# Optimization experiments

Hardware: AMD Instinct MI355X
Metric: run time of the kernel (lower is better)

Reference implementation:

```python
import jax, jax.numpy as jnp
import numpy as np

N, E = 2048, 65536
EMBED, H0, H1 = 64, 128, 128
VOCAB = 625  # 5**k with k=4
SLOPE = 0.01  # F.leaky_relu_ default negative slope


def setup_inputs() -> dict:
    key = jax.random.key(0)
    ks = jax.random.split(key, 20)
    f = jax.random.normal
    return {
        "node_ids": jax.random.randint(ks[0], (N,), 0, VOCAB),
        "edge_index": jax.random.randint(ks[1], (2, E), 0, N),
        "edge_attr": jax.random.uniform(ks[2], (E, 1), dtype=jnp.float32),
        "m": (jax.random.uniform(ks[3], (N, N)) > 0.5).astype(jnp.float32),
        "emb": f(ks[4], (VOCAB, EMBED), dtype=jnp.float32) * 0.1,
        "l0_lin1": f(ks[5], (H0, EMBED + 1), dtype=jnp.float32) * 0.1,
        "l0_lin2": f(ks[6], (H0, H0), dtype=jnp.float32) * 0.1,
        "l0_att_l": f(ks[7], (H0,), dtype=jnp.float32) * 0.1,
        "l0_att_r": f(ks[8], (EMBED,), dtype=jnp.float32) * 0.1,
        "l0_bias": f(ks[9], (H0,), dtype=jnp.float32) * 0.1,
        "l1_lin1": f(ks[10], (H1, H0 + 1), dtype=jnp.float32) * 0.1,
        "l1_lin2": f(ks[11], (H1, H1), dtype=jnp.float32) * 0.1,
        "l1_att_l": f(ks[12], (H1,), dtype=jnp.float32) * 0.1,
        "l1_att_r": f(ks[13], (H0,), dtype=jnp.float32) * 0.1,
        "l1_bias": f(ks[14], (H1,), dtype=jnp.float32) * 0.1,
        "W1": f(ks[15], (20, (EMBED + H0 + H1) * 2), dtype=jnp.float32) * 0.1,
        "b1": f(ks[16], (20,), dtype=jnp.float32) * 0.1,
        "W2": f(ks[17], (20,), dtype=jnp.float32) * 0.1,
        "b2": f(ks[18], (1,), dtype=jnp.float32) * 0.1,
    }


def _segment_softmax(alpha, index, n):
    # numerically-stable softmax over edges grouped by destination node
    amax = jax.ops.segment_max(alpha, index, num_segments=n)
    amax = jnp.where(jnp.isfinite(amax), amax, 0.0)
    e = jnp.exp(alpha - amax[index])
    denom = jax.ops.segment_sum(e, index, num_segments=n)
    return e / (denom[index] + 1e-16)


def _gate_conv(x, src, dst, edge_attr, lin1, lin2, att_l, att_r, bias, n):
    # PyG AttentiveFP GATEConv: message = lin2(leaky_relu(lin1([x_j, e]))) * alpha
    h = jax.nn.leaky_relu(jnp.concatenate([x[src], edge_attr], axis=-1) @ lin1.T, SLOPE)  # [E,out]
    alpha = jax.nn.leaky_relu(h @ att_l + x[dst] @ att_r, SLOPE)  # [E]
    alpha = _segment_softmax(alpha, dst, n)
    msg = (h @ lin2.T) * alpha[:, None]
    return jax.ops.segment_sum(msg, dst, num_segments=n) + bias


def reference(node_ids, edge_index, edge_attr, m, emb,
              l0_lin1, l0_lin2, l0_att_l, l0_att_r, l0_bias,
              l1_lin1, l1_lin2, l1_att_l, l1_att_r, l1_bias,
              W1, b1, W2, b2):
    src, dst = edge_index[0], edge_index[1]
    x = emb[node_ids]  # [N, EMBED]
    h1 = jax.nn.relu(_gate_conv(x, src, dst, edge_attr, l0_lin1, l0_lin2, l0_att_l, l0_att_r, l0_bias, N))
    h2 = jax.nn.relu(_gate_conv(h1, src, dst, edge_attr, l1_lin1, l1_lin2, l1_att_l, l1_att_r, l1_bias, N))
    feat = jnp.concatenate([x, h1, h2], axis=-1)  # [N, C], C = EMBED+H0+H1
    C = feat.shape[-1]
    # 1x1 conv over concat([x_i, x_j]) == split linear: out[c,i,j] = W1[c,:C]@feat[i] + W1[c,C:]@feat[j] + b1[c]
    a = feat @ W1[:, :C].T  # [N, 20] row (i) term
    b = feat @ W1[:, C:].T  # [N, 20] col (j) term
    h = jax.nn.relu(a[:, None, :] + b[None, :, :] + b1)  # [N, N, 20]
    logits = (h @ W2 + b2[0]) * m  # [N, N]; mask multiplies logits as in original
    return jax.nn.softmax(logits, axis=1)
```

## Files before the change

### kernel.cpp

```cpp
#include <hip/hip_runtime.h>
#include <math.h>

#define N 2048
#define E 65536
#define EMBED 64
#define H 128
#define NT 20
#define C3 320
#define CAP 96
#define SLOPE 0.01f

__device__ __forceinline__ float leaky(float x) { return x > 0.f ? x : SLOPE * x; }

__device__ __forceinline__ float wave_sum(float v) {
#pragma unroll
    for (int o = 32; o > 0; o >>= 1) v += __shfl_xor(v, o, 64);
    return v;
}

__global__ __launch_bounds__(256) void k_prep(
    const int* __restrict__ ei, const float* __restrict__ eattr,
    int* __restrict__ cursor, int* __restrict__ srcs, float* __restrict__ eas,
    const float* __restrict__ l1_lin1, float* __restrict__ WT1,
    const float* __restrict__ l0_lin2, float* __restrict__ LT0,
    const float* __restrict__ l1_lin2, float* __restrict__ LT1,
    const int* __restrict__ ids, const float* __restrict__ emb,
    const float* __restrict__ l0_lin1,
    float* __restrict__ x, float* __restrict__ A) {
    int b = blockIdx.x;
    int tid = threadIdx.x;
    if (b < 256) {
        int e = b * 256 + tid;
        int d = ei[E + e];
        int pos = atomicAdd(&cursor[d], 1);
        if (pos < CAP) {
            srcs[d * CAP + pos] = ei[e];
            eas[d * CAP + pos] = eattr[e];
        }
    } else if (b < 448) {
        int j = (b - 256) * 256 + tid;
        if (j < 16384) {
            int c = j >> 7, k = j & 127;
            WT1[j] = l1_lin1[k * (H + 1) + c];
        } else if (j < 32768) {
            int jj = j - 16384; int c = jj >> 7, k = jj & 127;
            LT0[jj] = l0_lin2[k * H + c];
        } else {
            int jj = j - 32768; int c = jj >> 7, k = jj & 127;
            LT1[jj] = l1_lin2[k * H + c];
        }
    } else {
        __shared__ float lw[EMBED][130];
        int n0 = (b - 448) * 8;
        for (int j = tid; j < H * (EMBED + 1); j += 256) {
            int k = j / (EMBED + 1), c = j % (EMBED + 1);
            float v = l0_lin1[j];
            if (c < EMBED) lw[c][k] = v;
        }
        for (int idx = tid; idx < 8 * EMBED; idx += 256) {
            int g = idx >> 6, c = idx & 63;
            x[(n0 + g) * EMBED + c] = emb[ids[n0 + g] * EMBED + c];
        }
        __syncthreads();
        int k = tid & 127, half = tid >> 7;
        const float* xr[4];
#pragma unroll
        for (int it = 0; it < 4; it++) {
            int nn = __builtin_amdgcn_readfirstlane(n0 + 2 * it + half);
            xr[it] = emb + (size_t)ids[nn] * EMBED;
        }
        float acc[4] = {0.f, 0.f, 0.f, 0.f};
#pragma unroll 4
        for (int c = 0; c < EMBED; c++) {
            float wt = lw[c][k];
#pragma unroll
            for (int it = 0; it < 4; it++) acc[it] = fmaf(xr[it][c], wt, acc[it]);
        }
#pragma unroll
        for (int it = 0; it < 4; it++) A[(n0 + 2 * it + half) * H + k] = acc[it];
    }
}

__device__ __forceinline__ void gate_wave(
    int dst, int lane, float xr,
    const float* __restrict__ A,
    float w0, float w1, float attl0, float attl1,
    const int* __restrict__ srcs, const float* __restrict__ eas, int cnt,
    float& out0, float& out1) {
    int c0 = 2 * lane;
    int base = dst * CAP;
    float mmax = -INFINITY, s = 0.f, v0 = 0.f, v1 = 0.f;
    for (int i0 = 0; i0 < cnt; i0 += 8) {
        int nb = cnt - i0; if (nb > 8) nb = 8;
        float h0[8], h1[8], p[8];
#pragma unroll
        for (int e = 0; e < 8; e++) {
            float ea = 0.f; float2 av = make_float2(0.f, 0.f);
            if (e < nb) {
                int sn = srcs[base + i0 + e];
                ea = eas[base + i0 + e];
                av = *(const float2*)&A[sn * H + c0];
            }
            h0[e] = leaky(fmaf(w0, ea, av.x));
            h1[e] = leaky(fmaf(w1, ea, av.y));
            p[e] = h0[e] * attl0 + h1[e] * attl1;
        }
#pragma unroll
        for (int o = 32; o > 0; o >>= 1) {
#pragma unroll
            for (int e = 0; e < 8; e++) p[e] += __shfl_xor(p[e], o, 64);
        }
        float alpha[8];
#pragma unroll
        for (int e = 0; e < 8; e++)
            alpha[e] = (e < nb) ? leaky(p[e] + xr) : -INFINITY;
        float mb = alpha[0];
#pragma unroll
        for (int e = 1; e < 8; e++) mb = fmaxf(mb, alpha[e]);
        float mnew = fmaxf(mmax, mb);
        float scale = __expf(mmax - mnew);
        float sw = 0.f, sv0 = 0.f, sv1 = 0.f;
#pragma unroll
        for (int e = 0; e < 8; e++) {
            float we = __expf(alpha[e] - mnew);
            sw += we;
            sv0 = fmaf(we, h0[e], sv0);
            sv1 = fmaf(we, h1[e], sv1);
        }
        s = fmaf(s, scale, sw);
        v0 = fmaf(v0, scale, sv0);
        v1 = fmaf(v1, scale, sv1);
        mmax = mnew;
    }
    float inv = 1.f / (s + 1e-16f);
    out0 = v0 * inv;
    out1 = v1 * inv;
}

__global__ __launch_bounds__(512) void k_g0(
    const float* __restrict__ x, const float* __restrict__ A0,
    const float* __restrict__ l0_lin1,
    const float* __restrict__ att_l, const float* __restrict__ att_r,
    const int* __restrict__ srcs, const float* __restrict__ eas,
    const int* __restrict__ cursor,
    const float* __restrict__ LT0, const float* __restrict__ b0,
    const float* __restrict__ WT1,
    float* __restrict__ h1, float* __restrict__ A1) {
    __shared__ float agg_s[8][H];
    __shared__ float hs[8][H];
    int n0 = blockIdx.x * 8;
    int tid = threadIdx.x;
    int wv = __builtin_amdgcn_readfirstlane(tid >> 6);
    int lane = tid & 63;
    int c0 = 2 * lane;

    int dst = n0 + wv;
    float xr = wave_sum(x[dst * EMBED + lane] * att_r[lane]);
    float attl0 = att_l[c0], attl1 = att_l[c0 + 1];
    float w0 = l0_lin1[c0 * (EMBED + 1) + EMBED];
    float w1 = l0_lin1[(c0 + 1) * (EMBED + 1) + EMBED];
    int cnt = cursor[dst]; if (cnt > CAP) cnt = CAP;

    float o0, o1;
    gate_wave(dst, lane, xr, A0, w0, w1, attl0, attl1, srcs, eas, cnt, o0, o1);
    agg_s[wv][c0] = o0;
    agg_s[wv][c0 + 1] = o1;
    __syncthreads();

    int k = tid & 127, q = tid >> 7;
    float bk = b0[k];
    float acc0 = bk, acc1 = bk;
#pragma unroll 4
    for (int c = 0; c < H; c++) {
        float wt = LT0[c * H + k];
        acc0 = fmaf(agg_s[q][c], wt, acc0);
        acc1 = fmaf(agg_s[q + 4][c], wt, acc1);
    }
    float hv0 = fmaxf(acc0, 0.f), hv1 = fmaxf(acc1, 0.f);
    h1[(n0 + q) * H + k] = hv0;
    h1[(n0 + q + 4) * H + k] = hv1;
    hs[q][k] = hv0;
    hs[q + 4][k] = hv1;
    __syncthreads();

    float a0 = 0.f, a1 = 0.f;
#pragma unroll 2
    for (int ct = 0; ct < H / 4; ct++) {
        float u0 = WT1[(4 * ct + 0) * H + k];
        float u1 = WT1[(4 * ct + 1) * H + k];
        float u2 = WT1[(4 * ct + 2) * H + k];
        float u3 = WT1[(4 * ct + 3) * H + k];
        float4 f0 = *(const float4*)&hs[q][4 * ct];
        float4 f1 = *(const float4*)&hs[q + 4][4 * ct];
        a0 = fmaf(f0.x, u0, a0); a0 = fmaf(f0.y, u1, a0);
        a0 = fmaf(f0.z, u2, a0); a0 = fmaf(f0.w, u3, a0);
        a1 = fmaf(f1.x, u0, a1); a1 = fmaf(f1.y, u1, a1);
        a1 = fmaf(f1.z, u2, a1); a1 = fmaf(f1.w, u3, a1);
    }
    A1[(n0 + q) * H + k] = a0;
    A1[(n0 + q + 4) * H + k] = a1;
}

__global__ __launch_bounds__(512) void k_g1(
    const float* __restrict__ h1g, const float* __restrict__ A1,
    const float* __restrict__ l1_lin1,
    const float* __restrict__ att_l, const float* __restrict__ att_r,
    const int* __restrict__ srcs, const float* __restrict__ eas,
    const int* __restrict__ cursor,
    const float* __restrict__ LT1, const float* __restrict__ bL1,
    const float* __restrict__ x, const float* __restrict__ W1,
    float* __restrict__ aArr, float* __restrict__ bT) {
    __shared__ float agg_s[8][H];
    __shared__ float feat[8][C3];
    int n0 = blockIdx.x * 8;
    int tid = threadIdx.x;
    int wv = __builtin_amdgcn_readfirstlane(tid >> 6);
    int lane = tid & 63;
    int c0 = 2 * lane;

    int dst = n0 + wv;
    float xr = wave_sum(h1g[dst * H + lane] * att_r[lane] +
                        h1g[dst * H + 64 + lane] * att_r[64 + lane]);
    float attl0 = att_l[c0], attl1 = att_l[c0 + 1];
    float w0 = l1_lin1[c0 * (H + 1) + H];
    float w1 = l1_lin1[(c0 + 1) * (H + 1) + H];
    int cnt = cursor[dst]; if (cnt > CAP) cnt = CAP;

    float o0, o1;
    gate_wave(dst, lane, xr, A1, w0, w1, attl0, attl1, srcs, eas, cnt, o0, o1);
    agg_s[wv][c0] = o0;
    agg_s[wv][c0 + 1] = o1;

    for (int idx = tid; idx < 8 * EMBED; idx += 512) {
        int g = idx >> 6, c = idx & 63;
        feat[g][c] = x[(n0 + g) * EMBED + c];
    }
    for (int idx = tid; idx < 8 * H; idx += 512) {
        int g = idx >> 7, c = idx & 127;
        feat[g][EMBED + c] = h1g[(n0 + g) * H + c];
    }
    __syncthreads();

    int k = tid & 127, q = tid >> 7;
    float bk = bL1[k];
    float acc0 = bk, acc1 = bk;
#pragma unroll 4
    for (int c = 0; c < H; c++) {
        float wt = LT1[c * H + k];
        acc0 = fmaf(agg_s[q][c], wt, acc0);
        acc1 = fmaf(agg_s[q + 4][c], wt, acc1);
    }
    feat[q][EMBED + H + k] = fmaxf(acc0, 0.f);
    feat[q + 4][EMBED + H + k] = fmaxf(acc1, 0.f);
    __syncthreads();

    if (tid < 320) {
        int g = tid / 40, u = tid % 40;
        int t = u % 20, side = u / 20;
        const float* wrow = W1 + t * (2 * C3) + side * C3;
        float s = 0.f;
#pragma unroll 4
        for (int ct = 0; ct < C3 / 4; ct++) {
            float4 fv = *(const float4*)&feat[g][4 * ct];
            float4 wv4 = *(const float4*)&wrow[4 * ct];
            s = fmaf(fv.x, wv4.x, s);
            s = fmaf(fv.y, wv4.y, s);
            s = fmaf(fv.z, wv4.z, s);
            s = fmaf(fv.w, wv4.w, s);
        }
        if (side == 0) aArr[(n0 + g) * NT + t] = s;
        else bT[t * N + (n0 + g)] = s;
    }
}

__global__ __launch_bounds__(256) void k_final(const float* __restrict__ aArr,
                                               const float* __restrict__ bT,
                                               const float* __restrict__ b1,
                                               const float* __restrict__ W2,
                                               const float* __restrict__ b2,
                                               const float* __restrict__ mmat,
                                               float* __restrict__ out) {
    __shared__ float lg[4][N];
    __shared__ float ash[4][NT];
    __shared__ float red[16];
    int i0 = blockIdx.x * 4;
    int tid = threadIdx.x;
    int wv = tid >> 6;
    if (tid < 4 * NT) ash[tid / NT][tid % NT] = aArr[i0 * NT + tid];
    float w2r[NT], b1r[NT];
#pragma unroll
    for (int t = 0; t < NT; t++) { w2r[t] = W2[t]; b1r[t] = b1[t]; }
    float b2v = b2[0];
    __syncthreads();

    float tmax[4] = {-INFINITY, -INFINITY, -INFINITY, -INFINITY};
    for (int j = tid; j < N; j += 256) {
        float bt[NT];
#pragma unroll
        for (int t = 0; t < NT; t++) bt[t] = bT[t * N + j];
#pragma unroll
        for (int g = 0; g < 4; g++) {
            float l = b2v;
#pragma unroll
            for (int t = 0; t < NT; t++)
                l += fmaxf(ash[g][t] + bt[t] + b1r[t], 0.f) * w2r[t];
            l *= mmat[(size_t)(i0 + g) * N + j];
            lg[g][j] = l;
            tmax[g] = fmaxf(tmax[g], l);
        }
    }
#pragma unroll
    for (int g = 0; g < 4; g++) {
#pragma unroll
        for (int o = 32; o > 0; o >>= 1) tmax[g] = fmaxf(tmax[g], __shfl_xor(tmax[g], o, 64));
    }
    if ((tid & 63) == 0) {
#pragma unroll
        for (int g = 0; g < 4; g++) red[wv * 4 + g] = tmax[g];
    }
    __syncthreads();
    float mfin[4];
#pragma unroll
    for (int g = 0; g < 4; g++)
        mfin[g] = fmaxf(fmaxf(red[g], red[4 + g]), fmaxf(red[8 + g], red[12 + g]));
    __syncthreads();

    float ts[4] = {0.f, 0.f, 0.f, 0.f};
    for (int j = tid; j < N; j += 256) {
#pragma unroll
        for (int g = 0; g < 4; g++) {
            float e = __expf(lg[g][j] - mfin[g]);
            lg[g][j] = e;
            ts[g] += e;
        }
    }
#pragma unroll
    for (int g = 0; g < 4; g++) {
#pragma unroll
        for (int o = 32; o > 0; o >>= 1) ts[g] += __shfl_xor(ts[g], o, 64);
    }
    if ((tid & 63) == 0) {
#pragma unroll
        for (int g = 0; g < 4; g++) red[wv * 4 + g] = ts[g];
    }
    __syncthreads();
    float inv[4];
#pragma unroll
    for (int g = 0; g < 4; g++)
        inv[g] = 1.f / (red[g] + red[4 + g] + red[8 + g] + red[12 + g]);

    for (int j = tid; j < N; j += 256) {
#pragma unroll
        for (int g = 0; g < 4; g++)
            out[(size_t)(i0 + g) * N + j] = lg[g][j] * inv[g];
    }
}

extern "C" void kernel_launch(void* const* d_in, const int* in_sizes, int n_in,
                              void* d_out, int out_size, void* d_ws, size_t ws_size,
                              hipStream_t stream) {
    const int*   node_ids = (const int*)d_in[0];
    const int*   ei       = (const int*)d_in[1];
    const float* eattr    = (const float*)d_in[2];
    const float* mmat     = (const float*)d_in[3];
    const float* emb      = (const float*)d_in[4];
    const float* l0_lin1  = (const float*)d_in[5];
    const float* l0_lin2  = (const float*)d_in[6];
    const float* l0_att_l = (const float*)d_in[7];
    const float* l0_att_r = (const float*)d_in[8];
    const float* l0_bias  = (const float*)d_in[9];
    const float* l1_lin1  = (const float*)d_in[10];
    const float* l1_lin2  = (const float*)d_in[11];
    const float* l1_att_l = (const float*)d_in[12];
    const float* l1_att_r = (const float*)d_in[13];
    const float* l1_bias  = (const float*)d_in[14];
    const float* W1       = (const float*)d_in[15];
    const float* b1       = (const float*)d_in[16];
    const float* W2       = (const float*)d_in[17];
    const float* b2       = (const float*)d_in[18];
    float* out = (float*)d_out;

    char* w = (char*)d_ws;
    auto alloc = [&](size_t bytes) {
        char* p = w;
        w += (bytes + 255) & ~(size_t)255;
        return p;
    };
    int*   cursor = (int*)alloc(N * sizeof(int));
    int*   srcs   = (int*)alloc(N * CAP * sizeof(int));
    float* eas    = (float*)alloc(N * CAP * sizeof(float));
    float* x      = (float*)alloc(N * EMBED * sizeof(float));
    float* A0     = (float*)alloc(N * H * sizeof(float));
    float* A1     = (float*)alloc(N * H * sizeof(float));
    float* h1     = (float*)alloc(N * H * sizeof(float));
    float* aArr   = (float*)alloc(N * NT * sizeof(float));
    float* bT     = (float*)alloc(NT * N * sizeof(float));
    float* WT1    = (float*)alloc(H * H * sizeof(float));
    float* LT0    = (float*)alloc(H * H * sizeof(float));
    float* LT1    = (float*)alloc(H * H * sizeof(float));

    hipMemsetAsync(cursor, 0, N * sizeof(int), stream);

    k_prep<<<704, 256, 0, stream>>>(ei, eattr, cursor, srcs, eas,
                                    l1_lin1, WT1, l0_lin2, LT0, l1_lin2, LT1,
                                    node_ids, emb, l0_lin1, x, A0);
    k_g0<<<N / 8, 512, 0, stream>>>(x, A0, l0_lin1, l0_att_l, l0_att_r,
                                    srcs, eas, cursor, LT0, l0_bias, WT1, h1, A1);
    k_g1<<<N / 8, 512, 0, stream>>>(h1, A1, l1_lin1, l1_att_l, l1_att_r,
                                    srcs, eas, cursor, LT1, l1_bias, x, W1, aArr, bT);
    k_final<<<N / 4, 256, 0, stream>>>(aArr, bT, b1, W2, b2, mmat, out);
}
```

Measured before the change: 193.8 us.

## Fuse all stages into one cooperative persistent kernel with grid syncs

Replaces the memset and four separate kernel launches with a single cooperative kernel of 512 blocks, 256 threads each, that separates stages with grid.sync(). Each block now handles 4 nodes instead of 8, and the cursor zeroing moves inside the kernel. The goal is to remove launch overhead and inter-kernel gaps. In exchange it adds grid-wide barrier costs, lowers per-block parallelism, and requires all 512 blocks to be co-resident, with launch_bounds(256,2) used to help that.

```diff
diff --git a/kernel.cpp b/kernel.cpp
--- a/kernel.cpp
+++ b/kernel.cpp
@@ -1,5 +1,8 @@
 #include <hip/hip_runtime.h>
+#include <hip/hip_cooperative_groups.h>
 #include <math.h>
+
+namespace cg = cooperative_groups;
 
 #define N 2048
 #define E 65536
@@ -16,69 +19,6 @@
 #pragma unroll
     for (int o = 32; o > 0; o >>= 1) v += __shfl_xor(v, o, 64);
     return v;
-}
-
-__global__ __launch_bounds__(256) void k_prep(
-    const int* __restrict__ ei, const float* __restrict__ eattr,
-    int* __restrict__ cursor, int* __restrict__ srcs, float* __restrict__ eas,
-    const float* __restrict__ l1_lin1, float* __restrict__ WT1,
-    const float* __restrict__ l0_lin2, float* __restrict__ LT0,
-    const float* __restrict__ l1_lin2, float* __restrict__ LT1,
-    const int* __restrict__ ids, const float* __restrict__ emb,
-    const float* __restrict__ l0_lin1,
-    float* __restrict__ x, float* __restrict__ A) {
-    int b = blockIdx.x;
-    int tid = threadIdx.x;
-    if (b < 256) {
-        int e = b * 256 + tid;
-        int d = ei[E + e];
-        int pos = atomicAdd(&cursor[d], 1);
-        if (pos < CAP) {
-            srcs[d * CAP + pos] = ei[e];
-            eas[d * CAP + pos] = eattr[e];
-        }
-    } else if (b < 448) {
-        int j = (b - 256) * 256 + tid;
-        if (j < 16384) {
-            int c = j >> 7, k = j & 127;
-            WT1[j] = l1_lin1[k * (H + 1) + c];
-        } else if (j < 32768) {
-            int jj = j - 16384; int c = jj >> 7, k = jj & 127;
-            LT0[jj] = l0_lin2[k * H + c];
-        } else {
-            int jj = j - 32768; int c = jj >> 7, k = jj & 127;
-            LT1[jj] = l1_lin2[k * H + c];
-        }
-    } else {
-        __shared__ float lw[EMBED][130];
-        int n0 = (b - 448) * 8;
-        for (int j = tid; j < H * (EMBED + 1); j += 256) {
-            int k = j / (EMBED + 1), c = j % (EMBED + 1);
-            float v = l0_lin1[j];
-            if (c < EMBED) lw[c][k] = v;
-        }
-        for (int idx = tid; idx < 8 * EMBED; idx += 256) {
-            int g = idx >> 6, c = idx & 63;
-            x[(n0 + g) * EMBED + c] = emb[ids[n0 + g] * EMBED + c];
-        }
-        __syncthreads();
-        int k = tid & 127, half = tid >> 7;
-        const float* xr[4];
-#pragma unroll
-        for (int it = 0; it < 4; it++) {
-            int nn = __builtin_amdgcn_readfirstlane(n0 + 2 * it + half);
-            xr[it] = emb + (size_t)ids[nn] * EMBED;
-        }
-        float acc[4] = {0.f, 0.f, 0.f, 0.f};
-#pragma unroll 4
-        for (int c = 0; c < EMBED; c++) {
-            float wt = lw[c][k];
-#pragma unroll
-            for (int it = 0; it < 4; it++) acc[it] = fmaf(xr[it][c], wt, acc[it]);
-        }
-#pragma unroll
-        for (int it = 0; it < 4; it++) A[(n0 + 2 * it + half) * H + k] = acc[it];
-    }
 }
 
 __device__ __forceinline__ void gate_wave(
@@ -137,222 +77,272 @@
     out1 = v1 * inv;
 }
 
-__global__ __launch_bounds__(512) void k_g0(
-    const float* __restrict__ x, const float* __restrict__ A0,
-    const float* __restrict__ l0_lin1,
-    const float* __restrict__ att_l, const float* __restrict__ att_r,
-    const int* __restrict__ srcs, const float* __restrict__ eas,
-    const int* __restrict__ cursor,
-    const float* __restrict__ LT0, const float* __restrict__ b0,
-    const float* __restrict__ WT1,
-    float* __restrict__ h1, float* __restrict__ A1) {
-    __shared__ float agg_s[8][H];
-    __shared__ float hs[8][H];
-    int n0 = blockIdx.x * 8;
+__global__ __launch_bounds__(256, 2) void k_fused(
+    const int* __restrict__ ei, const float* __restrict__ eattr,
+    const int* __restrict__ ids, const float* __restrict__ emb,
+    const float* __restrict__ l0_lin1, const float* __restrict__ l0_att_l,
+    const float* __restrict__ l0_att_r, const float* __restrict__ l0_bias,
+    const float* __restrict__ l1_lin1, const float* __restrict__ l1_att_l,
+    const float* __restrict__ l1_att_r, const float* __restrict__ l1_bias,
+    const float* __restrict__ l0_lin2, const float* __restrict__ l1_lin2,
+    const float* __restrict__ W1, const float* __restrict__ b1,
+    const float* __restrict__ W2, const float* __restrict__ b2,
+    const float* __restrict__ mmat, float* __restrict__ out,
+    int* __restrict__ cursor, int* __restrict__ srcs, float* __restrict__ eas,
+    float* __restrict__ x, float* __restrict__ A0, float* __restrict__ A1,
+    float* __restrict__ h1g, float* __restrict__ WT1, float* __restrict__ LT0,
+    float* __restrict__ LT1, float* __restrict__ aArr, float* __restrict__ bT) {
+    cg::grid_group grid = cg::this_grid();
+    __shared__ float smem[8352];
+    int b = blockIdx.x;
     int tid = threadIdx.x;
-    int wv = __builtin_amdgcn_readfirstlane(tid >> 6);
     int lane = tid & 63;
-    int c0 = 2 * lane;
-
-    int dst = n0 + wv;
-    float xr = wave_sum(x[dst * EMBED + lane] * att_r[lane]);
-    float attl0 = att_l[c0], attl1 = att_l[c0 + 1];
-    float w0 = l0_lin1[c0 * (EMBED + 1) + EMBED];
-    float w1 = l0_lin1[(c0 + 1) * (EMBED + 1) + EMBED];
-    int cnt = cursor[dst]; if (cnt > CAP) cnt = CAP;
-
-    float o0, o1;
-    gate_wave(dst, lane, xr, A0, w0, w1, attl0, attl1, srcs, eas, cnt, o0, o1);
-    agg_s[wv][c0] = o0;
-    agg_s[wv][c0 + 1] = o1;
-    __syncthreads();
-
-    int k = tid & 127, q = tid >> 7;
-    float bk = b0[k];
-    float acc0 = bk, acc1 = bk;
+    int n4 = b * 4;
+
+    {
+        int j = b * 256 + tid;
+        if (j < 2048) cursor[j] = 0;
+        int j2 = j - 2048;
+        if (j2 >= 0 && j2 < 16384) {
+            int c = j2 >> 7, k = j2 & 127;
+            WT1[j2] = l1_lin1[k * (H + 1) + c];
+        } else if (j2 >= 16384 && j2 < 32768) {
+            int jj = j2 - 16384; int c = jj >> 7, k = jj & 127;
+            LT0[jj] = l0_lin2[k * H + c];
+        } else if (j2 >= 32768 && j2 < 49152) {
+            int jj = j2 - 32768; int c = jj >> 7, k = jj & 127;
+            LT1[jj] = l1_lin2[k * H + c];
+        }
+        float* lw = smem;
+        for (int jj = tid; jj < H * (EMBED + 1); jj += 256) {
+            int k = jj / (EMBED + 1), c = jj % (EMBED + 1);
+            float v = l0_lin1[jj];
+            if (c < EMBED) lw[c * 130 + k] = v;
+        }
+        for (int idx = tid; idx < 4 * EMBED; idx += 256) {
+            int g = idx >> 6, c = idx & 63;
+            x[(n4 + g) * EMBED + c] = emb[ids[n4 + g] * EMBED + c];
+        }
+        __syncthreads();
+        int k = tid & 127, half = tid >> 7;
+        const float* xr_[2];
+#pragma unroll
+        for (int it = 0; it < 2; it++) {
+            int nn = __builtin_amdgcn_readfirstlane(n4 + 2 * it + half);
+            xr_[it] = emb + (size_t)ids[nn] * EMBED;
+        }
+        float acc[2] = {0.f, 0.f};
 #pragma unroll 4
-    for (int c = 0; c < H; c++) {
-        float wt = LT0[c * H + k];
-        acc0 = fmaf(agg_s[q][c], wt, acc0);
-        acc1 = fmaf(agg_s[q + 4][c], wt, acc1);
-    }
-    float hv0 = fmaxf(acc0, 0.f), hv1 = fmaxf(acc1, 0.f);
-    h1[(n0 + q) * H + k] = hv0;
-    h1[(n0 + q + 4) * H + k] = hv1;
-    hs[q][k] = hv0;
-    hs[q + 4][k] = hv1;
-    __syncthreads();
-
-    float a0 = 0.f, a1 = 0.f;
+        for (int c = 0; c < EMBED; c++) {
+            float wt = lw[c * 130 + k];
+            acc[0] = fmaf(xr_[0][c], wt, acc[0]);
+            acc[1] = fmaf(xr_[1][c], wt, acc[1]);
+        }
+        A0[(n4 + half) * H + k] = acc[0];
+        A0[(n4 + 2 + half) * H + k] = acc[1];
+    }
+    grid.sync();
+
+    {
+        int e = b * 256 + tid;
+        if (e < E) {
+            int d = ei[E + e];
+            int pos = atomicAdd(&cursor[d], 1);
+            if (pos < CAP) {
+                srcs[d * CAP + pos] = ei[e];
+                eas[d * CAP + pos] = eattr[e];
+            }
+        }
+    }
+    grid.sync();
+
+    {
+        float* agg_s = smem;
+        float* hs = smem + 512;
+        int wv = __builtin_amdgcn_readfirstlane(tid >> 6);
+        int c0 = 2 * lane;
+        int dst = n4 + wv;
+        float xr = wave_sum(x[dst * EMBED + lane] * l0_att_r[lane]);
+        float attl0 = l0_att_l[c0], attl1 = l0_att_l[c0 + 1];
+        float w0 = l0_lin1[c0 * (EMBED + 1) + EMBED];
+        float w1 = l0_lin1[(c0 + 1) * (EMBED + 1) + EMBED];
+        int cnt = cursor[dst]; if (cnt > CAP) cnt = CAP;
+        float o0, o1;
+        gate_wave(dst, lane, xr, A0, w0, w1, attl0, attl1, srcs, eas, cnt, o0, o1);
+        agg_s[wv * H + c0] = o0;
+        agg_s[wv * H + c0 + 1] = o1;
+        __syncthreads();
+
+        int k = tid & 127, q = tid >> 7;
+        float bk = l0_bias[k];
+        float acc0 = bk, acc1 = bk;
+#pragma unroll 4
+        for (int c = 0; c < H; c++) {
+            float wt = LT0[c * H + k];
+            acc0 = fmaf(agg_s[q * H + c], wt, acc0);
+            acc1 = fmaf(agg_s[(q + 2) * H + c], wt, acc1);
+        }
+        float hv0 = fmaxf(acc0, 0.f), hv1 = fmaxf(acc1, 0.f);
+        h1g[(n4 + q) * H + k] = hv0;
+        h1g[(n4 + q + 2) * H + k] = hv1;
+        hs[q * H + k] = hv0;
+        hs[(q + 2) * H + k] = hv1;
+        __syncthreads();
+
+        float a0 = 0.f, a1 = 0.f;
 #pragma unroll 2
-    for (int ct = 0; ct < H / 4; ct++) {
-        float u0 = WT1[(4 * ct + 0) * H + k];
-        float u1 = WT1[(4 * ct + 1) * H + k];
-        float u2 = WT1[(4 * ct + 2) * H + k];
-        float u3 = WT1[(4 * ct + 3) * H + k];
-        float4 f0 = *(const float4*)&hs[q][4 * ct];
-        float4 f1 = *(const float4*)&hs[q + 4][4 * ct];
-        a0 = fmaf(f0.x, u0, a0); a0 = fmaf(f0.y, u1, a0);
-        a0 = fmaf(f0.z, u2, a0); a0 = fmaf(f0.w, u3, a0);
-        a1 = fmaf(f1.x, u0, a1); a1 = fmaf(f1.y, u1, a1);
-        a1 = fmaf(f1.z, u2, a1); a1 = fmaf(f1.w, u3, a1);
-    }
-    A1[(n0 + q) * H + k] = a0;
-    A1[(n0 + q + 4) * H + k] = a1;
-}
-
-__global__ __launch_bounds__(512) void k_g1(
-    const float* __restrict__ h1g, const float* __restrict__ A1,
-    const float* __restrict__ l1_lin1,
-    const float* __restrict__ att_l, const float* __restrict__ att_r,
-    const int* __restrict__ srcs, const float* __restrict__ eas,
-    const int* __restrict__ cursor,
-    const float* __restrict__ LT1, const float* __restrict__ bL1,
-    const float* __restrict__ x, const float* __restrict__ W1,
-    float* __restrict__ aArr, float* __restrict__ bT) {
-    __shared__ float agg_s[8][H];
-    __shared__ float feat[8][C3];
-    int n0 = blockIdx.x * 8;
-    int tid = threadIdx.x;
-    int wv = __builtin_amdgcn_readfirstlane(tid >> 6);
-    int lane = tid & 63;
-    int c0 = 2 * lane;
-
-    int dst = n0 + wv;
-    float xr = wave_sum(h1g[dst * H + lane] * att_r[lane] +
-                        h1g[dst * H + 64 + lane] * att_r[64 + lane]);
-    float attl0 = att_l[c0], attl1 = att_l[c0 + 1];
-    float w0 = l1_lin1[c0 * (H + 1) + H];
-    float w1 = l1_lin1[(c0 + 1) * (H + 1) + H];
-    int cnt = cursor[dst]; if (cnt > CAP) cnt = CAP;
-
-    float o0, o1;
-    gate_wave(dst, lane, xr, A1, w0, w1, attl0, attl1, srcs, eas, cnt, o0, o1);
-    agg_s[wv][c0] = o0;
-    agg_s[wv][c0 + 1] = o1;
-
-    for (int idx = tid; idx < 8 * EMBED; idx += 512) {
-        int g = idx >> 6, c = idx & 63;
-        feat[g][c] = x[(n0 + g) * EMBED + c];
-    }
-    for (int idx = tid; idx < 8 * H; idx += 512) {
-        int g = idx >> 7, c = idx & 127;
-        feat[g][EMBED + c] = h1g[(n0 + g) * H + c];
-    }
-    __syncthreads();
-
-    int k = tid & 127, q = tid >> 7;
-    float bk = bL1[k];
-    float acc0 = bk, acc1 = bk;
+        for (int ct = 0; ct < H / 4; ct++) {
+            float u0 = WT1[(4 * ct + 0) * H + k];
+            float u1 = WT1[(4 * ct + 1) * H + k];
+            float u2 = WT1[(4 * ct + 2) * H + k];
+            float u3 = WT1[(4 * ct + 3) * H + k];
+            float4 f0 = *(const float4*)&hs[q * H + 4 * ct];
+            float4 f1 = *(const float4*)&hs[(q + 2) * H + 4 * ct];
+            a0 = fmaf(f0.x, u0, a0); a0 = fmaf(f0.y, u1, a0);
+            a0 = fmaf(f0.z, u2, a0); a0 = fmaf(f0.w, u3, a0);
+            a1 = fmaf(f1.x, u0, a1); a1 = fmaf(f1.y, u1, a1);
+            a1 = fmaf(f1.z, u2, a1); a1 = fmaf(f1.w, u3, a1);
+        }
+        A1[(n4 + q) * H + k] = a0;
+        A1[(n4 + q + 2) * H + k] = a1;
+    }
+    grid.sync();
+
+    {
+        float* agg_s = smem;
+        float* feat = smem + 512;
+        int wv = __builtin_amdgcn_readfirstlane(tid >> 6);
+        int c0 = 2 * lane;
+        int dst = n4 + wv;
+        float xr = wave_sum(h1g[dst * H + lane] * l1_att_r[lane] +
+                            h1g[dst * H + 64 + lane] * l1_att_r[64 + lane]);
+        float attl0 = l1_att_l[c0], attl1 = l1_att_l[c0 + 1];
+        float w0 = l1_lin1[c0 * (H + 1) + H];
+        float w1 = l1_lin1[(c0 + 1) * (H + 1) + H];
+        int cnt = cursor[dst]; if (cnt > CAP) cnt = CAP;
+        float o0, o1;
+        gate_wave(dst, lane, xr, A1, w0, w1, attl0, attl1, srcs, eas, cnt, o0, o1);
+        agg_s[wv * H + c0] = o0;
+        agg_s[wv * H + c0 + 1] = o1;
+        for (int idx = tid; idx < 4 * EMBED; idx += 256) {
+            int g = idx >> 6, c = idx & 63;
+            feat[g * C3 + c] = x[(n4 + g) * EMBED + c];
+        }
+        for (int idx = tid; idx < 4 * H; idx += 256) {
+            int g = idx >> 7, c = idx & 127;
+            feat[g * C3 + EMBED + c] = h1g[(n4 + g) * H + c];
+        }
+        __syncthreads();
+
+        int k = tid & 127, q = tid >> 7;
+        float bk = l1_bias[k];
+        float acc0 = bk, acc1 = bk;
 #pragma unroll 4
-    for (int c = 0; c < H; c++) {
-        float wt = LT1[c * H + k];
-        acc0 = fmaf(agg_s[q][c], wt, acc0);
-        acc1 = fmaf(agg_s[q + 4][c], wt, acc1);
-    }
-    feat[q][EMBED + H + k] = fmaxf(acc0, 0.f);
-    feat[q + 4][EMBED + H + k] = fmaxf(acc1, 0.f);
-    __syncthreads();
-
-    if (tid < 320) {
-        int g = tid / 40, u = tid % 40;
-        int t = u % 20, side = u / 20;
-        const float* wrow = W1 + t * (2 * C3) + side * C3;
-        float s = 0.f;
+        for (int c = 0; c < H; c++) {
+            float wt = LT1[c * H + k];
+            acc0 = fmaf(agg_s[q * H + c], wt, acc0);
+            acc1 = fmaf(agg_s[(q + 2) * H + c], wt, acc1);
+        }
+        feat[q * C3 + EMBED + H + k] = fmaxf(acc0, 0.f);
+        feat[(q + 2) * C3 + EMBED + H + k] = fmaxf(acc1, 0.f);
+        __syncthreads();
+
+        if (tid < 4 * 2 * NT) {
+            int g = tid / 40, u = tid % 40;
+            int t = u % 20, side = u / 20;
+            const float* wrow = W1 + t * (2 * C3) + side * C3;
+            const float* fv = feat + g * C3;
+            float s = 0.f;
 #pragma unroll 4
-        for (int ct = 0; ct < C3 / 4; ct++) {
-            float4 fv = *(const float4*)&feat[g][4 * ct];
-            float4 wv4 = *(const float4*)&wrow[4 * ct];
-            s = fmaf(fv.x, wv4.x, s);
-            s = fmaf(fv.y, wv4.y, s);
-            s = fmaf(fv.z, wv4.z, s);
-            s = fmaf(fv.w, wv4.w, s);
-        }
-        if (side == 0) aArr[(n0 + g) * NT + t] = s;
-        else bT[t * N + (n0 + g)] = s;
-    }
-}
-
-__global__ __launch_bounds__(256) void k_final(const float* __restrict__ aArr,
-                                               const float* __restrict__ bT,
-                                               const float* __restrict__ b1,
-                                               const float* __restrict__ W2,
-                                               const float* __restrict__ b2,
-                                               const float* __restrict__ mmat,
-                                               float* __restrict__ out) {
-    __shared__ float lg[4][N];
-    __shared__ float ash[4][NT];
-    __shared__ float red[16];
-    int i0 = blockIdx.x * 4;
-    int tid = threadIdx.x;
-    int wv = tid >> 6;
-    if (tid < 4 * NT) ash[tid / NT][tid % NT] = aArr[i0 * NT + tid];
-    float w2r[NT], b1r[NT];
-#pragma unroll
-    for (int t = 0; t < NT; t++) { w2r[t] = W2[t]; b1r[t] = b1[t]; }
-    float b2v = b2[0];
-    __syncthreads();
-
-    float tmax[4] = {-INFINITY, -INFINITY, -INFINITY, -INFINITY};
-    for (int j = tid; j < N; j += 256) {
-        float bt[NT];
-#pragma unroll
-        for (int t = 0; t < NT; t++) bt[t] = bT[t * N + j];
+            for (int ct = 0; ct < C3 / 4; ct++) {
+                float4 f4 = *(const float4*)&fv[4 * ct];
+                float4 w4 = *(const float4*)&wrow[4 * ct];
+                s = fmaf(f4.x, w4.x, s);
+                s = fmaf(f4.y, w4.y, s);
+                s = fmaf(f4.z, w4.z, s);
+                s = fmaf(f4.w, w4.w, s);
+            }
+            if (side == 0) aArr[(n4 + g) * NT + t] = s;
+            else bT[t * N + (n4 + g)] = s;
+        }
+    }
+    grid.sync();
+
+    {
+        float* lg = smem;
+        float* ash = smem + 8192;
+        float* red = smem + 8272;
+        int i0 = b * 4;
+        int wv = tid >> 6;
+        if (tid < 4 * NT) ash[tid] = aArr[i0 * NT + tid];
+        float w2r[NT], b1r[NT];
+#pragma unroll
+        for (int t = 0; t < NT; t++) { w2r[t] = W2[t]; b1r[t] = b1[t]; }
+        float b2v = b2[0];
+        __syncthreads();
+
+        float tmax[4] = {-INFINITY, -INFINITY, -INFINITY, -INFINITY};
+        for (int j = tid; j < N; j += 256) {
+            float bt[NT];
+#pragma unroll
+            for (int t = 0; t < NT; t++) bt[t] = bT[t * N + j];
+#pragma unroll
+            for (int g = 0; g < 4; g++) {
+                float l = b2v;
+#pragma unroll
+                for (int t = 0; t < NT; t++)
+                    l += fmaxf(ash[g * NT + t] + bt[t] + b1r[t], 0.f) * w2r[t];
+                l *= mmat[(size_t)(i0 + g) * N + j];
+                lg[g * N + j] = l;
+                tmax[g] = fmaxf(tmax[g], l);
+            }
+        }
 #pragma unroll
         for (int g = 0; g < 4; g++) {
-            float l = b2v;
-#pragma unroll
-            for (int t = 0; t < NT; t++)
-                l += fmaxf(ash[g][t] + bt[t] + b1r[t], 0.f) * w2r[t];
-            l *= mmat[(size_t)(i0 + g) * N + j];
-            lg[g][j] = l;
-            tmax[g] = fmaxf(tmax[g], l);
-        }
-    }
-#pragma unroll
-    for (int g = 0; g < 4; g++) {
-#pragma unroll
-        for (int o = 32; o > 0; o >>= 1) tmax[g] = fmaxf(tmax[g], __shfl_xor(tmax[g], o, 64));
-    }
-    if ((tid & 63) == 0) {
-#pragma unroll
-        for (int g = 0; g < 4; g++) red[wv * 4 + g] = tmax[g];
-    }
-    __syncthreads();
-    float mfin[4];
-#pragma unroll
-    for (int g = 0; g < 4; g++)
-        mfin[g] = fmaxf(fmaxf(red[g], red[4 + g]), fmaxf(red[8 + g], red[12 + g]));
-    __syncthreads();
-
-    float ts[4] = {0.f, 0.f, 0.f, 0.f};
-    for (int j = tid; j < N; j += 256) {
+#pragma unroll
+            for (int o = 32; o > 0; o >>= 1)
+                tmax[g] = fmaxf(tmax[g], __shfl_xor(tmax[g], o, 64));
+        }
+        if (lane == 0) {
+#pragma unroll
+            for (int g = 0; g < 4; g++) red[wv * 4 + g] = tmax[g];
+        }
+        __syncthreads();
+        float mfin[4];
+#pragma unroll
+        for (int g = 0; g < 4; g++)
+            mfin[g] = fmaxf(fmaxf(red[g], red[4 + g]), fmaxf(red[8 + g], red[12 + g]));
+        __syncthreads();
+
+        float ts[4] = {0.f, 0.f, 0.f, 0.f};
+        for (int j = tid; j < N; j += 256) {
+#pragma unroll
+            for (int g = 0; g < 4; g++) {
+                float e = __expf(lg[g * N + j] - mfin[g]);
+                lg[g * N + j] = e;
+                ts[g] += e;
+            }
+        }
 #pragma unroll
         for (int g = 0; g < 4; g++) {
-            float e = __expf(lg[g][j] - mfin[g]);
-            lg[g][j] = e;
-            ts[g] += e;
-        }
-    }
-#pragma unroll
-    for (int g = 0; g < 4; g++) {
-#pragma unroll
-        for (int o = 32; o > 0; o >>= 1) ts[g] += __shfl_xor(ts[g], o, 64);
-    }
-    if ((tid & 63) == 0) {
-#pragma unroll
-        for (int g = 0; g < 4; g++) red[wv * 4 + g] = ts[g];
-    }
-    __syncthreads();
-    float inv[4];
-#pragma unroll
-    for (int g = 0; g < 4; g++)
-        inv[g] = 1.f / (red[g] + red[4 + g] + red[8 + g] + red[12 + g]);
-
-    for (int j = tid; j < N; j += 256) {
+#pragma unroll
+            for (int o = 32; o > 0; o >>= 1) ts[g] += __shfl_xor(ts[g], o, 64);
+        }
+        if (lane == 0) {
+#pragma unroll
+            for (int g = 0; g < 4; g++) red[wv * 4 + g] = ts[g];
+        }
+        __syncthreads();
+        float inv[4];
 #pragma unroll
         for (int g = 0; g < 4; g++)
-            out[(size_t)(i0 + g) * N + j] = lg[g][j] * inv[g];
+            inv[g] = 1.f / (red[g] + red[4 + g] + red[8 + g] + red[12 + g]);
+
+        for (int j = tid; j < N; j += 256) {
+#pragma unroll
+            for (int g = 0; g < 4; g++)
+                out[(size_t)(i0 + g) * N + j] = lg[g * N + j] * inv[g];
+        }
     }
 }
 
@@ -399,14 +389,18 @@
     float* LT0    = (float*)alloc(H * H * sizeof(float));
     float* LT1    = (float*)alloc(H * H * sizeof(float));
 
-    hipMemsetAsync(cursor, 0, N * sizeof(int), stream);
-
-    k_prep<<<704, 256, 0, stream>>>(ei, eattr, cursor, srcs, eas,
-                                    l1_lin1, WT1, l0_lin2, LT0, l1_lin2, LT1,
-                                    node_ids, emb, l0_lin1, x, A0);
-    k_g0<<<N / 8, 512, 0, stream>>>(x, A0, l0_lin1, l0_att_l, l0_att_r,
-                                    srcs, eas, cursor, LT0, l0_bias, WT1, h1, A1);
-    k_g1<<<N / 8, 512, 0, stream>>>(h1, A1, l1_lin1, l1_att_l, l1_att_r,
-                                    srcs, eas, cursor, LT1, l1_bias, x, W1, aArr, bT);
-    k_final<<<N / 4, 256, 0, stream>>>(aArr, bT, b1, W2, b2, mmat, out);
+    void* args[] = {
+        (void*)&ei, (void*)&eattr, (void*)&node_ids, (void*)&emb,
+        (void*)&l0_lin1, (void*)&l0_att_l, (void*)&l0_att_r, (void*)&l0_bias,
+        (void*)&l1_lin1, (void*)&l1_att_l, (void*)&l1_att_r, (void*)&l1_bias,
+        (void*)&l0_lin2, (void*)&l1_lin2,
+        (void*)&W1, (void*)&b1, (void*)&W2, (void*)&b2,
+        (void*)&mmat, (void*)&out,
+        (void*)&cursor, (void*)&srcs, (void*)&eas,
+        (void*)&x, (void*)&A0, (void*)&A1, (void*)&h1,
+        (void*)&WT1, (void*)&LT0, (void*)&LT1,
+        (void*)&aArr, (void*)&bT,
+    };
+    hipLaunchCooperativeKernel((const void*)k_fused, dim3(512), dim3(256),
+                               args, 0, stream);
 }
```

Result: slower. 435.7 us (+124.9%).
